# Performance work log

Measured on AMD Instinct MI355X. Metric: run time of the kernel, lower is better.

The kernel has to match this reference:

```python
import jax, jax.numpy as jnp
import numpy as np

DIM = 1024
NUM_HEADS = 8  # only used for the scale; heads are never actually split
SCALE = float((DIM // NUM_HEADS) ** 0.5)


def _attn(x, wq, wk, wv):
    # Single-head full-dim attention, faithful to the source (no head split).
    Q = x @ wq.T  # [B,S,D]
    K = x @ wk.T
    V = x @ wv.T
    scores = jnp.einsum('bqd,bkd->bqk', Q, K) / SCALE  # [B,S,S]
    attn = jax.nn.softmax(scores, axis=-1)
    return jnp.einsum('bqk,bkd->bqd', attn, V)


def setup_inputs() -> dict:
    key = jax.random.key(0)
    ks = jax.random.split(key, 9)
    B, S, D = 4, 2048, DIM
    w = lambda k: jax.random.normal(k, (D, D), dtype=jnp.float32) * 0.02
    return {
        'x': jax.random.normal(ks[0], (B, S, D), dtype=jnp.float32),
        'wq1': w(ks[1]), 'wk1': w(ks[2]), 'wv1': w(ks[3]),
        'fc1_w': w(ks[4]),
        'wq2': w(ks[5]), 'wk2': w(ks[6]), 'wv2': w(ks[7]),
        'fc2_w': w(ks[8]),
    }


def reference(x, wq1, wk1, wv1, fc1_w, wq2, wk2, wv2, fc2_w):
    h = _attn(x, wq1, wk1, wv1)
    h = jax.nn.silu(h)
    h = h @ fc1_w.T
    h = _attn(h, wq2, wk2, wv2)
    h = jax.nn.silu(h)
    h = h @ fc2_w.T
    return jax.nn.softmax(h, axis=-1)
```

## Files before the change

kernel.cpp:

```cpp
#include <hip/hip_runtime.h>
#include <math.h>


typedef __attribute__((ext_vector_type(8))) int i32x8;
typedef __attribute__((ext_vector_type(4))) int i32x4;
typedef __attribute__((ext_vector_type(4))) float f32x4;
typedef unsigned char u8;
typedef unsigned int u32;

#define EPI_F8 1
#define EPI_QKV 2
#define EPI_EXP 3
#define EPI_PV 4
#define EPI_EXPF32 5

__device__ __forceinline__ void gload_lds16(const void* g, void* l) {
    __builtin_amdgcn_global_load_lds(
        (const __attribute__((address_space(1))) void*)g,
        (__attribute__((address_space(3))) void*)l, 16, 0, 0);
}

__device__ __forceinline__ u8 cvt_f8(float v) {
    return (u8)(__builtin_amdgcn_cvt_pk_fp8_f32(v, v, 0, false) & 0xFF);
}

template <int EPI>
__global__ __launch_bounds__(256) void gemm_fp8(
    const u8* __restrict__ A, const u8* __restrict__ B,
    void* __restrict__ C0, void* __restrict__ C1, void* __restrict__ C2,
    int K, int ldA, int ldB, int ldC,
    long long bsA, long long bsB, long long bsC, float alpha, float beta)
{
    __shared__ u8 sA[128 * 128];
    __shared__ u8 sB[128 * 128];

    const int tid = threadIdx.x;
    const int wave = tid >> 6, lane = tid & 63;
    const int wm = wave >> 1, wn = wave & 1;
    const int m0 = blockIdx.y * 128, n0 = blockIdx.x * 128;
    const long long z = blockIdx.z;

    const u8* pA = A + z * bsA;
    const u8* pB = B + z * bsB;

    int blkid[4], rs_[4], cs16[4];
#pragma unroll
    for (int i = 0; i < 4; i++) {
        blkid[i] = wave * 256 + i * 64 + lane;
        rs_[i] = blkid[i] >> 3;
        cs16[i] = ((blkid[i] & 7) ^ (rs_[i] & 7)) * 16;
    }

    f32x4 acc[4][4] = {};
    const int fr = lane & 15, fc2 = (lane >> 4) * 2;

    for (int k0 = 0; k0 < K; k0 += 128) {
#pragma unroll
        for (int i = 0; i < 4; i++) {
            gload_lds16(pA + (long long)(m0 + rs_[i]) * ldA + k0 + cs16[i],
                        sA + blkid[i] * 16);
            gload_lds16(pB + (long long)(n0 + rs_[i]) * ldB + k0 + cs16[i],
                        sB + blkid[i] * 16);
        }
        __syncthreads();

        i32x8 a[4], b[4];
#pragma unroll
        for (int i = 0; i < 4; i++) {
            const int row = wm * 64 + i * 16 + fr;
            const int sw = row & 7;
            i32x4 lo = *(const i32x4*)(sA + row * 128 + ((fc2 + 0) ^ sw) * 16);
            i32x4 hi = *(const i32x4*)(sA + row * 128 + ((fc2 + 1) ^ sw) * 16);
            a[i] = __builtin_shufflevector(lo, hi, 0, 1, 2, 3, 4, 5, 6, 7);
        }
#pragma unroll
        for (int j = 0; j < 4; j++) {
            const int row = wn * 64 + j * 16 + fr;
            const int sw = row & 7;
            i32x4 lo = *(const i32x4*)(sB + row * 128 + ((fc2 + 0) ^ sw) * 16);
            i32x4 hi = *(const i32x4*)(sB + row * 128 + ((fc2 + 1) ^ sw) * 16);
            b[j] = __builtin_shufflevector(lo, hi, 0, 1, 2, 3, 4, 5, 6, 7);
        }
#pragma unroll
        for (int i = 0; i < 4; i++)
#pragma unroll
            for (int j = 0; j < 4; j++)
                acc[i][j] = __builtin_amdgcn_mfma_scale_f32_16x16x128_f8f6f4(
                    a[i], b[j], acc[i][j], 0 , 0 ,
                    0, 0x7F7F7F7F, 0, 0x7F7F7F7F);
        __syncthreads();
    }

    const int col = lane & 15;
    const int rbase = (lane >> 4) * 4;

    if (EPI == EPI_EXP || EPI == EPI_EXPF32) {
        u8* P = (u8*)C0 + z * bsC;
        float* Cw = (float*)C0 + z * bsC;
        float* rsum = (EPI == EPI_EXP) ? ((float*)C1 + z * 2048) : (float*)C1;
#pragma unroll
        for (int i = 0; i < 4; i++) {
            const int mloc0 = m0 + wm * 64 + i * 16 + rbase;
            float rowp[4] = {0.f, 0.f, 0.f, 0.f};
#pragma unroll
            for (int j = 0; j < 4; j++) {
                const int nloc = n0 + wn * 64 + j * 16 + col;
#pragma unroll
                for (int r = 0; r < 4; r++) {
                    float e = __expf(acc[i][j][r] * alpha);
                    rowp[r] += e;
                    if (EPI == EPI_EXP)
                        P[(long long)(mloc0 + r) * ldC + nloc] =
                            cvt_f8(e * 0.0625f);
                    else
                        Cw[(long long)(mloc0 + r) * ldC + nloc] = e;
                }
            }
#pragma unroll
            for (int r = 0; r < 4; r++) {
                float t = rowp[r];
                t += __shfl_xor(t, 1);
                t += __shfl_xor(t, 2);
                t += __shfl_xor(t, 4);
                t += __shfl_xor(t, 8);
                if ((lane & 15) == 0) atomicAdd(&rsum[mloc0 + r], t);
            }
        }
        return;
    }

#pragma unroll
    for (int i = 0; i < 4; i++) {
        const int mloc0 = m0 + wm * 64 + i * 16 + rbase;
        float inv[4];
        if (EPI == EPI_PV) {
            const float* rsum = (const float*)C1 + z * 2048;
#pragma unroll
            for (int r = 0; r < 4; r++) inv[r] = alpha / rsum[mloc0 + r];
        }
#pragma unroll
        for (int j = 0; j < 4; j++) {
            const int nloc = n0 + wn * 64 + j * 16 + col;
            if (EPI == EPI_F8) {
                u8* C = (u8*)C0 + z * bsC;
#pragma unroll
                for (int r = 0; r < 4; r++)
                    C[(long long)(mloc0 + r) * ldC + nloc] =
                        cvt_f8(acc[i][j][r] * alpha);
            } else if (EPI == EPI_PV) {
                u8* C = (u8*)C0 + z * bsC;
#pragma unroll
                for (int r = 0; r < 4; r++) {
                    float v = acc[i][j][r] * inv[r];
                    v = v / (1.f + __expf(-v));
                    C[(long long)(mloc0 + r) * ldC + nloc] = cvt_f8(v * beta);
                }
            } else {
                const int seg = nloc >> 10;
                const int nn = nloc & 1023;
                float v[4];
#pragma unroll
                for (int r = 0; r < 4; r++) v[r] = acc[i][j][r] * alpha;
                if (seg == 2) {
                    const int bb = mloc0 >> 11, mm = mloc0 & 2047;
                    int p01 = __builtin_amdgcn_cvt_pk_fp8_f32(v[0], v[1], 0, false);
                    int p23 = __builtin_amdgcn_cvt_pk_fp8_f32(v[2], v[3], 0, false);
                    u32 pk = (u32)(p01 & 0xFFFF) | ((u32)p23 << 16);
                    *(u32*)((u8*)C2 + (long long)bb * (1024LL * 2048) +
                            (long long)nn * 2048 + mm) = pk;
                } else {
                    u8* C = seg ? (u8*)C1 : (u8*)C0;
#pragma unroll
                    for (int r = 0; r < 4; r++)
                        C[(long long)(mloc0 + r) * 1024 + nn] = cvt_f8(v[r]);
                }
            }
        }
    }
}

__global__ __launch_bounds__(256) void convert_all(
    const float* x, const float* w0, const float* w1, const float* w2,
    const float* w3, const float* w4, const float* w5, const float* w6,
    const float* w7, u8* __restrict__ ax, u8* __restrict__ wf,
    float* __restrict__ rz)
{
    const int bid = blockIdx.x;
    if (bid < 24) {
        float4 zero = {0.f, 0.f, 0.f, 0.f};
        *(float4*)(rz + ((long long)bid * 256 + threadIdx.x) * 4) = zero;
    }
    const float* src;
    u8* dst;
    float scale;
    long long i;
    if (bid < 8192) {
        src = x; dst = ax; scale = 8.f;
        i = ((long long)bid * 256 + threadIdx.x) * 4;
    } else {
        const float* ws[8] = {w0, w1, w2, w3, w4, w5, w6, w7};
        const int wi = (bid - 8192) >> 10;
        src = ws[wi]; scale = 256.f;
        dst = wf + (long long)wi * 1024 * 1024;
        i = (((long long)(bid - 8192) & 1023) * 256 + threadIdx.x) * 4;
    }
    float4 v = *(const float4*)(src + i);
    int p01 = __builtin_amdgcn_cvt_pk_fp8_f32(v.x * scale, v.y * scale, 0, false);
    int p23 = __builtin_amdgcn_cvt_pk_fp8_f32(v.z * scale, v.w * scale, 0, false);
    *(u32*)(dst + i) = (u32)(p01 & 0xFFFF) | ((u32)p23 << 16);
}

__global__ __launch_bounds__(256) void normalize_1024(
    const float* __restrict__ e, const float* __restrict__ rsum,
    float* __restrict__ out)
{
    const long long row = blockIdx.x;
    const float inv = 1.0f / rsum[row];
    const float* p = e + row * 1024;
    float* o = out + row * 1024;
    float4 v = *(const float4*)(p + threadIdx.x * 4);
    float4 ov;
    ov.x = v.x * inv; ov.y = v.y * inv; ov.z = v.z * inv; ov.w = v.w * inv;
    *(float4*)(o + threadIdx.x * 4) = ov;
}

extern "C" void kernel_launch(void* const* d_in, const int* in_sizes, int n_in,
                              void* d_out, int out_size, void* d_ws, size_t ws_size,
                              hipStream_t stream)
{
    float* out = (float*)d_out;

    constexpr int Bt = 4, S = 2048, D = 1024;
    constexpr int M = Bt * S;
    const long long MD = (long long)M * D;
    const long long DD = (long long)D * D;
    const long long SD = (long long)S * D;
    const long long SS = (long long)S * S;

    u8* Af = (u8*)d_ws;
    u8* Wf = Af + MD;
    u8* Qf = Wf + 8 * DD;
    u8* Kf = Qf + MD;
    u8* VT = Kf + MD;
    u8* Pf = VT + MD;
    u8* Hs = Pf + (long long)Bt * SS;
    float* SC = (float*)(Hs + MD);
    float* rsum0 = SC + MD;
    float* rsum1 = rsum0 + M;
    float* rsum2 = rsum1 + M;

    const dim3 blk(256);

    const float SOFT = 0.08838834764831845f;
    const float a_qkv[2] = {8.f / 2048.f, 1024.f / 65536.f};
    const float a_qk[2]  = {SOFT / 64.f, SOFT / 1048576.f};
    const float a_pv[2]  = {2.0f, 1.f / 64.f};
    const float b_pv[2]  = {256.f, 65536.f};
    const float a_fc[2]  = {256.f / 65536.f, 1.f / 16777216.f};

    convert_all<<<dim3(16384), blk, 0, stream>>>(
        (const float*)d_in[0], (const float*)d_in[1], (const float*)d_in[2],
        (const float*)d_in[3], (const float*)d_in[4], (const float*)d_in[5],
        (const float*)d_in[6], (const float*)d_in[7], (const float*)d_in[8],
        Af, Wf, rsum0);

    const dim3 gqkv(3 * D / 128, M / 128, 1);
    const dim3 gw(D / 128, M / 128, 1);
    const dim3 gqk(S / 128, S / 128, Bt);
    const dim3 gpv(D / 128, S / 128, Bt);

    for (int layer = 0; layer < 2; layer++) {
        const u8* wqkv = Wf + (long long)(layer * 4) * DD;
        const u8* fc   = Wf + (long long)(layer * 4 + 3) * DD;
        float* rsum    = layer ? rsum1 : rsum0;

        gemm_fp8<EPI_QKV><<<gqkv, blk, 0, stream>>>(
            Af, wqkv, Qf, Kf, VT, D, D, D, D, 0, 0, 0, a_qkv[layer], 0.f);
        gemm_fp8<EPI_EXP><<<gqk, blk, 0, stream>>>(
            Qf, Kf, Pf, rsum, nullptr, D, D, D, S, SD, SD, SS,
            a_qk[layer], 0.f);
        gemm_fp8<EPI_PV><<<gpv, blk, 0, stream>>>(
            Pf, VT, Hs, rsum, nullptr, S, S, S, D, SS, (long long)D * S, SD,
            a_pv[layer], b_pv[layer]);
        if (layer == 0) {
            gemm_fp8<EPI_F8><<<gw, blk, 0, stream>>>(
                Hs, fc, Af, nullptr, nullptr, D, D, D, D, 0, 0, 0,
                a_fc[0], 0.f);
        } else {
            gemm_fp8<EPI_EXPF32><<<gw, blk, 0, stream>>>(
                Hs, fc, SC, rsum2, nullptr, D, D, D, D, 0, 0, 0,
                a_fc[1], 0.f);
        }
    }

    normalize_1024<<<dim3(M), blk, 0, stream>>>(SC, rsum2, out);
}
```

Baseline: 352.8 us.

## Compute transposed GEMMs by swapping operands so epilogues store packed contiguous rows

Every GEMM now computes C^T by swapping the A and B operands and the grid axes. Each lane's four accumulator values then fall on consecutive output columns, so the epilogues write packed 4-byte fp8 words or float4 stores instead of scattered single bytes or floats. Row-sum reductions become cross-lane shuffles over lanes 16 and 32. The V-transpose path now writes single bytes instead of the previous packed store, trading one layout for another.

```diff
diff --git a/kernel.cpp b/kernel.cpp
--- a/kernel.cpp
+++ b/kernel.cpp
@@ -22,6 +22,12 @@
 
 __device__ __forceinline__ u8 cvt_f8(float v) {
     return (u8)(__builtin_amdgcn_cvt_pk_fp8_f32(v, v, 0, false) & 0xFF);
+}
+
+__device__ __forceinline__ u32 pack_f8x4(float v0, float v1, float v2, float v3) {
+    int p01 = __builtin_amdgcn_cvt_pk_fp8_f32(v0, v1, 0, false);
+    int p23 = __builtin_amdgcn_cvt_pk_fp8_f32(v2, v3, 0, false);
+    return (u32)(p01 & 0xFFFF) | ((u32)p23 << 16);
 }
 
 template <int EPI>
@@ -94,85 +100,99 @@
     const int col = lane & 15;
     const int rbase = (lane >> 4) * 4;
 
-    if (EPI == EPI_EXP || EPI == EPI_EXPF32) {
+    if (EPI == EPI_EXP) {
         u8* P = (u8*)C0 + z * bsC;
-        float* Cw = (float*)C0 + z * bsC;
-        float* rsum = (EPI == EPI_EXP) ? ((float*)C1 + z * 2048) : (float*)C1;
-#pragma unroll
-        for (int i = 0; i < 4; i++) {
-            const int mloc0 = m0 + wm * 64 + i * 16 + rbase;
-            float rowp[4] = {0.f, 0.f, 0.f, 0.f};
-#pragma unroll
-            for (int j = 0; j < 4; j++) {
-                const int nloc = n0 + wn * 64 + j * 16 + col;
-#pragma unroll
-                for (int r = 0; r < 4; r++) {
-                    float e = __expf(acc[i][j][r] * alpha);
-                    rowp[r] += e;
-                    if (EPI == EPI_EXP)
-                        P[(long long)(mloc0 + r) * ldC + nloc] =
-                            cvt_f8(e * 0.0625f);
-                    else
-                        Cw[(long long)(mloc0 + r) * ldC + nloc] = e;
-                }
+        float* rsum = (float*)C1 + z * 2048;
+#pragma unroll
+        for (int j = 0; j < 4; j++) {
+            const int Cq = n0 + wn * 64 + j * 16 + col;
+            float part = 0.f;
+#pragma unroll
+            for (int i = 0; i < 4; i++) {
+                const int R0 = m0 + wm * 64 + i * 16 + rbase;
+                float e0 = __expf(acc[i][j][0] * alpha);
+                float e1 = __expf(acc[i][j][1] * alpha);
+                float e2 = __expf(acc[i][j][2] * alpha);
+                float e3 = __expf(acc[i][j][3] * alpha);
+                part += (e0 + e1) + (e2 + e3);
+                *(u32*)(P + (long long)Cq * ldC + R0) =
+                    pack_f8x4(e0 * 0.0625f, e1 * 0.0625f,
+                              e2 * 0.0625f, e3 * 0.0625f);
             }
-#pragma unroll
-            for (int r = 0; r < 4; r++) {
-                float t = rowp[r];
-                t += __shfl_xor(t, 1);
-                t += __shfl_xor(t, 2);
-                t += __shfl_xor(t, 4);
-                t += __shfl_xor(t, 8);
-                if ((lane & 15) == 0) atomicAdd(&rsum[mloc0 + r], t);
+            part += __shfl_xor(part, 16);
+            part += __shfl_xor(part, 32);
+            if (lane < 16) atomicAdd(&rsum[Cq], part);
+        }
+        return;
+    }
+
+    if (EPI == EPI_EXPF32) {
+        float* Cw = (float*)C0;
+        float* rsum = (float*)C1;
+#pragma unroll
+        for (int j = 0; j < 4; j++) {
+            const int Cq = n0 + wn * 64 + j * 16 + col;
+            float part = 0.f;
+#pragma unroll
+            for (int i = 0; i < 4; i++) {
+                const int R0 = m0 + wm * 64 + i * 16 + rbase;
+                float4 e;
+                e.x = __expf(acc[i][j][0] * alpha);
+                e.y = __expf(acc[i][j][1] * alpha);
+                e.z = __expf(acc[i][j][2] * alpha);
+                e.w = __expf(acc[i][j][3] * alpha);
+                part += (e.x + e.y) + (e.z + e.w);
+                *(float4*)(Cw + (long long)Cq * ldC + R0) = e;
             }
+            part += __shfl_xor(part, 16);
+            part += __shfl_xor(part, 32);
+            if (lane < 16) atomicAdd(&rsum[Cq], part);
         }
         return;
     }
 
 #pragma unroll
-    for (int i = 0; i < 4; i++) {
-        const int mloc0 = m0 + wm * 64 + i * 16 + rbase;
-        float inv[4];
+    for (int j = 0; j < 4; j++) {
+        const int Cq = n0 + wn * 64 + j * 16 + col;
+        float inv;
         if (EPI == EPI_PV) {
             const float* rsum = (const float*)C1 + z * 2048;
-#pragma unroll
-            for (int r = 0; r < 4; r++) inv[r] = alpha / rsum[mloc0 + r];
-        }
-#pragma unroll
-        for (int j = 0; j < 4; j++) {
-            const int nloc = n0 + wn * 64 + j * 16 + col;
+            inv = alpha / rsum[Cq];
+        }
+#pragma unroll
+        for (int i = 0; i < 4; i++) {
+            const int R0 = m0 + wm * 64 + i * 16 + rbase;
             if (EPI == EPI_F8) {
                 u8* C = (u8*)C0 + z * bsC;
-#pragma unroll
-                for (int r = 0; r < 4; r++)
-                    C[(long long)(mloc0 + r) * ldC + nloc] =
-                        cvt_f8(acc[i][j][r] * alpha);
+                *(u32*)(C + (long long)Cq * ldC + R0) =
+                    pack_f8x4(acc[i][j][0] * alpha, acc[i][j][1] * alpha,
+                              acc[i][j][2] * alpha, acc[i][j][3] * alpha);
             } else if (EPI == EPI_PV) {
                 u8* C = (u8*)C0 + z * bsC;
+                float v[4];
 #pragma unroll
                 for (int r = 0; r < 4; r++) {
-                    float v = acc[i][j][r] * inv[r];
-                    v = v / (1.f + __expf(-v));
-                    C[(long long)(mloc0 + r) * ldC + nloc] = cvt_f8(v * beta);
+                    float t = acc[i][j][r] * inv;
+                    v[r] = (t / (1.f + __expf(-t))) * beta;
                 }
+                *(u32*)(C + (long long)Cq * ldC + R0) =
+                    pack_f8x4(v[0], v[1], v[2], v[3]);
             } else {
-                const int seg = nloc >> 10;
-                const int nn = nloc & 1023;
-                float v[4];
-#pragma unroll
-                for (int r = 0; r < 4; r++) v[r] = acc[i][j][r] * alpha;
+                const int seg = R0 >> 10;
+                const int db = R0 & 1023;
                 if (seg == 2) {
-                    const int bb = mloc0 >> 11, mm = mloc0 & 2047;
-                    int p01 = __builtin_amdgcn_cvt_pk_fp8_f32(v[0], v[1], 0, false);
-                    int p23 = __builtin_amdgcn_cvt_pk_fp8_f32(v[2], v[3], 0, false);
-                    u32 pk = (u32)(p01 & 0xFFFF) | ((u32)p23 << 16);
-                    *(u32*)((u8*)C2 + (long long)bb * (1024LL * 2048) +
-                            (long long)nn * 2048 + mm) = pk;
+                    const int bb = Cq >> 11, tt = Cq & 2047;
+                    u8* VTp = (u8*)C2;
+#pragma unroll
+                    for (int r = 0; r < 4; r++)
+                        VTp[(long long)bb * (1024LL * 2048) +
+                            (long long)(db + r) * 2048 + tt] =
+                            cvt_f8(acc[i][j][r] * alpha);
                 } else {
                     u8* C = seg ? (u8*)C1 : (u8*)C0;
-#pragma unroll
-                    for (int r = 0; r < 4; r++)
-                        C[(long long)(mloc0 + r) * 1024 + nn] = cvt_f8(v[r]);
+                    *(u32*)(C + (long long)Cq * 1024 + db) =
+                        pack_f8x4(acc[i][j][0] * alpha, acc[i][j][1] * alpha,
+                                  acc[i][j][2] * alpha, acc[i][j][3] * alpha);
                 }
             }
         }
@@ -205,9 +225,8 @@
         i = (((long long)(bid - 8192) & 1023) * 256 + threadIdx.x) * 4;
     }
     float4 v = *(const float4*)(src + i);
-    int p01 = __builtin_amdgcn_cvt_pk_fp8_f32(v.x * scale, v.y * scale, 0, false);
-    int p23 = __builtin_amdgcn_cvt_pk_fp8_f32(v.z * scale, v.w * scale, 0, false);
-    *(u32*)(dst + i) = (u32)(p01 & 0xFFFF) | ((u32)p23 << 16);
+    *(u32*)(dst + i) = pack_f8x4(v.x * scale, v.y * scale,
+                                 v.z * scale, v.w * scale);
 }
 
 __global__ __launch_bounds__(256) void normalize_1024(
@@ -264,10 +283,10 @@
         (const float*)d_in[6], (const float*)d_in[7], (const float*)d_in[8],
         Af, Wf, rsum0);
 
-    const dim3 gqkv(3 * D / 128, M / 128, 1);
-    const dim3 gw(D / 128, M / 128, 1);
+    const dim3 gqkv(M / 128, 3 * D / 128, 1);
     const dim3 gqk(S / 128, S / 128, Bt);
-    const dim3 gpv(D / 128, S / 128, Bt);
+    const dim3 gpv(S / 128, D / 128, Bt);
+    const dim3 gw(M / 128, D / 128, 1);
 
     for (int layer = 0; layer < 2; layer++) {
         const u8* wqkv = Wf + (long long)(layer * 4) * DD;
@@ -275,20 +294,20 @@
         float* rsum    = layer ? rsum1 : rsum0;
 
         gemm_fp8<EPI_QKV><<<gqkv, blk, 0, stream>>>(
-            Af, wqkv, Qf, Kf, VT, D, D, D, D, 0, 0, 0, a_qkv[layer], 0.f);
+            wqkv, Af, Qf, Kf, VT, D, D, D, D, 0, 0, 0, a_qkv[layer], 0.f);
         gemm_fp8<EPI_EXP><<<gqk, blk, 0, stream>>>(
-            Qf, Kf, Pf, rsum, nullptr, D, D, D, S, SD, SD, SS,
+            Kf, Qf, Pf, rsum, nullptr, D, D, D, S, SD, SD, SS,
             a_qk[layer], 0.f);
         gemm_fp8<EPI_PV><<<gpv, blk, 0, stream>>>(
-            Pf, VT, Hs, rsum, nullptr, S, S, S, D, SS, (long long)D * S, SD,
-            a_pv[layer], b_pv[layer]);
+            VT, Pf, Hs, rsum, nullptr, S, S, S, D,
+            (long long)D * S, SS, SD, a_pv[layer], b_pv[layer]);
         if (layer == 0) {
             gemm_fp8<EPI_F8><<<gw, blk, 0, stream>>>(
-                Hs, fc, Af, nullptr, nullptr, D, D, D, D, 0, 0, 0,
+                fc, Hs, Af, nullptr, nullptr, D, D, D, D, 0, 0, 0,
                 a_fc[0], 0.f);
         } else {
             gemm_fp8<EPI_EXPF32><<<gw, blk, 0, stream>>>(
-                Hs, fc, SC, rsum2, nullptr, D, D, D, D, 0, 0, 0,
+                fc, Hs, SC, rsum2, nullptr, D, D, D, D, 0, 0, 0,
                 a_fc[1], 0.f);
         }
     }
```

Measured after the change: 344.5 us. 1.02x faster.
